# Kernel tuning notes

Measured on AMD Instinct MI355X. Metric: run time of the kernel, lower is better.

The kernel has to match this reference:

```python
import jax, jax.numpy as jnp
import numpy as np


def setup_inputs() -> dict:
    key = jax.random.key(0)
    # Uniform in (0.9, 1.1) so the running product over 8192 elements stays finite.
    x = jax.random.uniform(key, (4096, 8192), dtype=jnp.float32, minval=0.9, maxval=1.1)
    return {"x": x}


def reference(x) -> jnp.ndarray:
    # Inclusive prefix product along dim 1 (matches cumprod_dim1_cuda / torch.cumprod(x, dim=1)).
    return jnp.cumprod(x, axis=1)
```

## Files before the change

### kernel.cpp

```cpp
#include <hip/hip_runtime.h>


#define N      8192
#define T      256
#define CHUNK  32

__global__ __launch_bounds__(T) void cumprod_rows_kernel(
    const float* __restrict__ x, float* __restrict__ out, int n_rows)
{
    __shared__ float wtot[T / 64];

    const int row = blockIdx.x;
    if (row >= n_rows) return;
    const int tid  = threadIdx.x;
    const int lane = tid & 63;
    const int wid  = tid >> 6;

    const float* __restrict__ xr   = x   + (size_t)row * N + (size_t)tid * CHUNK;
    float*       __restrict__ outr = out + (size_t)row * N + (size_t)tid * CHUNK;

    float vals[CHUNK];
    const float4* __restrict__ src = reinterpret_cast<const float4*>(xr);
#pragma unroll
    for (int i = 0; i < CHUNK / 4; ++i) {
        const float4 d = src[i];
        vals[4 * i + 0] = d.x; vals[4 * i + 1] = d.y;
        vals[4 * i + 2] = d.z; vals[4 * i + 3] = d.w;
    }

    float p = 1.0f;
#pragma unroll
    for (int j = 0; j < CHUNK; ++j) { p *= vals[j]; vals[j] = p; }

    float inc = p;
#pragma unroll
    for (int off = 1; off < 64; off <<= 1) {
        const float o = __shfl_up(inc, off, 64);
        if (lane >= off) inc *= o;
    }
    if (lane == 63) wtot[wid] = inc;
    __syncthreads();

    float excl = __shfl_up(inc, 1, 64);
    if (lane == 0) excl = 1.0f;
#pragma unroll
    for (int w = 0; w < T / 64; ++w)
        if (w < wid) excl *= wtot[w];

    float4* __restrict__ dst = reinterpret_cast<float4*>(outr);
#pragma unroll
    for (int i = 0; i < CHUNK / 4; ++i) {
        float4 d;
        d.x = vals[4 * i + 0] * excl; d.y = vals[4 * i + 1] * excl;
        d.z = vals[4 * i + 2] * excl; d.w = vals[4 * i + 3] * excl;
        dst[i] = d;
    }
}

extern "C" void kernel_launch(void* const* d_in, const int* in_sizes, int n_in,
                              void* d_out, int out_size, void* d_ws, size_t ws_size,
                              hipStream_t stream)
{
    const float* x   = (const float*)d_in[0];
    float*       out = (float*)d_out;
    const int n_rows = in_sizes[0] / N;
    cumprod_rows_kernel<<<n_rows, T, 0, stream>>>(x, out, n_rows);
}
```

Before: 238.1 us.

## Use coalesced warp-segment layout with per-segment wave scans for cumprod

Each thread previously owned 32 contiguous elements, so a wave's float4 loads were strided 128 bytes apart. Now each wave owns a contiguous quarter of the row, split into 8 segments of 256 elements. Lanes load consecutive float4s within each segment, so accesses are fully coalesced. The cost is 8 independent wave-level shuffle scans instead of one, plus a serial carry across segments. Launch bounds now request 6 blocks per CU to cap register use.

```diff
diff --git a/kernel.cpp b/kernel.cpp
--- a/kernel.cpp
+++ b/kernel.cpp
@@ -1,59 +1,83 @@
 #include <hip/hip_runtime.h>
 
 
-#define N      8192
-#define T      256
-#define CHUNK  32
+#define N     8192
+#define T     256
+#define NW    (T / 64)
+#define WE    (N / NW)
+#define SEGS  8
+#define SE    (WE / SEGS)
 
-__global__ __launch_bounds__(T) void cumprod_rows_kernel(
+__global__ __launch_bounds__(T, 6) void cumprod_rows_kernel(
     const float* __restrict__ x, float* __restrict__ out, int n_rows)
 {
-    __shared__ float wtot[T / 64];
+    __shared__ float wtot[NW];
 
-    const int row = blockIdx.x;
+    const int row  = blockIdx.x;
     if (row >= n_rows) return;
     const int tid  = threadIdx.x;
     const int lane = tid & 63;
     const int wid  = tid >> 6;
 
-    const float* __restrict__ xr   = x   + (size_t)row * N + (size_t)tid * CHUNK;
-    float*       __restrict__ outr = out + (size_t)row * N + (size_t)tid * CHUNK;
+    const size_t base = (size_t)row * N + (size_t)wid * WE + (size_t)lane * 4;
+    const float* __restrict__ xr   = x   + base;
+    float*       __restrict__ outr = out + base;
 
-    float vals[CHUNK];
-    const float4* __restrict__ src = reinterpret_cast<const float4*>(xr);
+    float v[SEGS][4];
 #pragma unroll
-    for (int i = 0; i < CHUNK / 4; ++i) {
-        const float4 d = src[i];
-        vals[4 * i + 0] = d.x; vals[4 * i + 1] = d.y;
-        vals[4 * i + 2] = d.z; vals[4 * i + 3] = d.w;
+    for (int s = 0; s < SEGS; ++s) {
+        const float4 d = *reinterpret_cast<const float4*>(xr + s * SE);
+        v[s][0] = d.x; v[s][1] = d.y; v[s][2] = d.z; v[s][3] = d.w;
     }
 
-    float p = 1.0f;
+    float linc[SEGS];
 #pragma unroll
-    for (int j = 0; j < CHUNK; ++j) { p *= vals[j]; vals[j] = p; }
+    for (int s = 0; s < SEGS; ++s) {
+        v[s][1] *= v[s][0];
+        v[s][2] *= v[s][1];
+        v[s][3] *= v[s][2];
+        linc[s] = v[s][3];
+    }
 
-    float inc = p;
 #pragma unroll
     for (int off = 1; off < 64; off <<= 1) {
-        const float o = __shfl_up(inc, off, 64);
-        if (lane >= off) inc *= o;
+#pragma unroll
+        for (int s = 0; s < SEGS; ++s) {
+            const float o = __shfl_up(linc[s], off, 64);
+            if (lane >= off) linc[s] *= o;
+        }
     }
-    if (lane == 63) wtot[wid] = inc;
+
+    float e[SEGS], t[SEGS];
+#pragma unroll
+    for (int s = 0; s < SEGS; ++s) {
+        t[s] = __shfl(linc[s], 63, 64);
+        float ee = __shfl_up(linc[s], 1, 64);
+        e[s] = (lane == 0) ? 1.0f : ee;
+    }
+
+    float carry = 1.0f;
+#pragma unroll
+    for (int s = 0; s < SEGS; ++s) {
+        e[s] *= carry;
+        carry *= t[s];
+    }
+
+    if (lane == 0) wtot[wid] = carry;
     __syncthreads();
 
-    float excl = __shfl_up(inc, 1, 64);
-    if (lane == 0) excl = 1.0f;
+    float wpre = 1.0f;
 #pragma unroll
-    for (int w = 0; w < T / 64; ++w)
-        if (w < wid) excl *= wtot[w];
+    for (int w = 0; w < NW; ++w)
+        if (w < wid) wpre *= wtot[w];
 
-    float4* __restrict__ dst = reinterpret_cast<float4*>(outr);
 #pragma unroll
-    for (int i = 0; i < CHUNK / 4; ++i) {
+    for (int s = 0; s < SEGS; ++s) {
+        const float m = e[s] * wpre;
         float4 d;
-        d.x = vals[4 * i + 0] * excl; d.y = vals[4 * i + 1] * excl;
-        d.z = vals[4 * i + 2] * excl; d.w = vals[4 * i + 3] * excl;
-        dst[i] = d;
+        d.x = v[s][0] * m; d.y = v[s][1] * m;
+        d.z = v[s][2] * m; d.w = v[s][3] * m;
+        *reinterpret_cast<float4*>(outr + s * SE) = d;
     }
 }
 
```

After: 230.2 us. -3.3%, faster.
